# Kernel optimization log

Measured on AMD Instinct MI355X. Metric: run time of the kernel, lower is better.

The kernel has to match this reference:

```python
import jax, jax.numpy as jnp
import numpy as np

B, L, F, P, E, H, D, C, V = 256, 100, 8, 4, 64, 4, 64, 32, 10000
HD = H * D  # 256 = att_dim * head_num
TOWER_IN = F * E + F * E + P * E + C  # 1312
LN_EPS = 1e-3  # keras LayerNormalization default epsilon


def _ln(x, g, b):
    m = jnp.mean(x, axis=-1, keepdims=True)
    v = jnp.mean(jnp.square(x - m), axis=-1, keepdims=True)
    return (x - m) * jax.lax.rsqrt(v + LN_EPS) * g + b


def setup_inputs() -> dict:
    key = jax.random.key(0)
    ks = jax.random.split(key, 32)
    w = lambda k, s: jax.random.normal(k, s, jnp.float32) * 0.02
    inp = {
        'target_ad': jax.random.randint(ks[0], (B, F), 0, V),
        'ubs_feature': jax.random.randint(ks[1], (B, L, F), 0, V),
        'profile_feature': jax.random.randint(ks[2], (B, P), 0, V),
        'context_feature': jax.random.normal(ks[3], (B, C), jnp.float32),
        # embedding tables: one per sparse feature, stacked
        'item_tables': w(ks[4], (F, V, E)),
        'profile_tables': w(ks[5], (P, V, E)),
        # per-timestep distinct attention weights, stacked over L
        'q_w': w(ks[6], (L, E, HD)),
        'k_w': w(ks[7], (L, E, HD)),
        'v_w': w(ks[8], (L, E, HD)),
        'lin_w': w(ks[9], (L, HD, E)),
        'lin_b': jnp.zeros((L, E), jnp.float32),
        # shared post-attention layernorm
        'ln_g': jnp.ones((E,), jnp.float32),
        'ln_b': jnp.zeros((E,), jnp.float32),
        # dense tower
        't_w1': w(ks[10], (TOWER_IN, 1024)), 't_b1': jnp.zeros((1024,), jnp.float32),
        't_g1': jnp.ones((1024,), jnp.float32), 't_bb1': jnp.zeros((1024,), jnp.float32),
        't_w2': w(ks[11], (1024, 512)), 't_b2': jnp.zeros((512,), jnp.float32),
        't_g2': jnp.ones((512,), jnp.float32), 't_bb2': jnp.zeros((512,), jnp.float32),
        't_w3': w(ks[12], (512, 256)), 't_b3': jnp.zeros((256,), jnp.float32),
        't_g3': jnp.ones((256,), jnp.float32), 't_bb3': jnp.zeros((256,), jnp.float32),
        't_w4': w(ks[13], (256, 1)), 't_b4': jnp.zeros((1,), jnp.float32),
    }
    return inp


def reference(target_ad, ubs_feature, profile_feature, context_feature,
              item_tables, profile_tables, q_w, k_w, v_w, lin_w, lin_b,
              ln_g, ln_b,
              t_w1, t_b1, t_g1, t_bb1,
              t_w2, t_b2, t_g2, t_bb2,
              t_w3, t_b3, t_g3, t_bb3,
              t_w4, t_b4):
    b = target_ad.shape[0]
    # embedding lookups (feature-wise tables)
    te = item_tables[jnp.arange(F)[None, :], target_ad]              # [B,F,E]
    ue = item_tables[jnp.arange(F)[None, None, :], ubs_feature]      # [B,L,F,E]
    pe = profile_tables[jnp.arange(P)[None, :], profile_feature]     # [B,P,E]

    # per-step distinct Q/K/V projections, batched over L via einsum
    q = jnp.einsum('blfe,leo->blfo', ue, q_w).reshape(b, L, F, H, D)
    k = jnp.einsum('blfe,leo->blfo', ue, k_w).reshape(b, L, F, H, D)
    v = jnp.einsum('blfe,leo->blfo', ue, v_w).reshape(b, L, F, H, D)
    scores = jnp.einsum('blfhd,blghd->blhfg', q, k) / jnp.sqrt(jnp.float32(D))
    attw = jax.nn.softmax(scores, axis=-1)                           # [B,L,H,F,F]
    att = jnp.einsum('blhfg,blghd->blfhd', attw, v).reshape(b, L, F, HD)
    att_out = jnp.einsum('blfo,loe->blfe', att, lin_w) + lin_b[None, :, None, :]
    # shared LayerNorm per step, summed over L (original accumulates into zeros_like)
    ubs_t = jnp.sum(_ln(att_out, ln_g, ln_b), axis=1)                # [B,F,E]
    ubs = jax.nn.relu(ubs_t / jnp.float32(L))

    total = jnp.concatenate([ubs.reshape(b, -1), te.reshape(b, -1),
                             pe.reshape(b, -1), context_feature], axis=-1)

    h = jax.nn.relu(_ln(total @ t_w1 + t_b1, t_g1, t_bb1))
    h = jax.nn.relu(_ln(h @ t_w2 + t_b2, t_g2, t_bb2))
    h = jax.nn.relu(_ln(h @ t_w3 + t_b3, t_g3, t_bb3))
    out = jax.nn.sigmoid(h @ t_w4 + t_b4)                            # [B,1]
    return out
```

## Files before the change

### kernel.cpp

```cpp
#include <hip/hip_runtime.h>
#include <hip/hip_bf16.h>

#define B_ 256
#define L_ 100
#define F_ 8
#define P_ 4
#define E_ 64
#define H_ 4
#define D_ 64
#define C_ 32
#define V_ 10000
#define TOWER_IN_ 1312
#define LN_EPS 0.001f
#define LCH_ 4
#define NCH_ 25
#define ZK_ 40

typedef __attribute__((ext_vector_type(8))) short bf8v;
typedef __attribute__((ext_vector_type(8))) unsigned short us8;
typedef __attribute__((ext_vector_type(4))) float f4v;

__device__ __forceinline__ unsigned short f2bf(float x) {
    __hip_bfloat16 h = __float2bfloat16(x);
    return __builtin_bit_cast(unsigned short, h);
}

#define BARRIER() do { \
    asm volatile("s_waitcnt lgkmcnt(0)" ::: "memory"); \
    __builtin_amdgcn_s_barrier(); \
    asm volatile("" ::: "memory"); \
} while (0)

__global__ __launch_bounds__(256) void precomp_kernel(
    const float* __restrict__ q_w, const float* __restrict__ k_w,
    const float* __restrict__ v_w, const float* __restrict__ lin_w,
    unsigned short* __restrict__ wsMT, unsigned short* __restrict__ wsWT)
{
    __shared__ float sA[64][65];
    __shared__ float sB[64][65];
    const int t = threadIdx.x;
    const int l = blockIdx.x >> 2;
    const int h = blockIdx.x & 3;
    const size_t obase = (size_t)(l * 4 + h) * 4096;

    for (int i = 0; i < 16; ++i) {
        int idx = t + i * 256;
        int e = idx >> 6, d = idx & 63;
        sA[e][d] = q_w[(l * 64 + e) * 256 + h * 64 + d];
        sB[e][d] = k_w[(l * 64 + e) * 256 + h * 64 + d];
    }
    __syncthreads();
    for (int i = 0; i < 16; ++i) {
        int idx = t + i * 256;
        int o = idx >> 6, e = idx & 63;
        float s = 0.f;
        #pragma unroll 8
        for (int d = 0; d < 64; ++d) s += sA[e][d] * sB[o][d];
        wsMT[obase + idx] = f2bf(s);
    }
    __syncthreads();

    for (int i = 0; i < 16; ++i) {
        int idx = t + i * 256;
        int dd = idx >> 6, oo = idx & 63;
        sB[dd][oo] = lin_w[l * 16384 + (h * 64 + dd) * 64 + oo];
    }
    for (int i = 0; i < 16; ++i) {
        int idx = t + i * 256;
        int e = idx >> 6, d = idx & 63;
        sA[e][d] = v_w[(l * 64 + e) * 256 + h * 64 + d];
    }
    __syncthreads();
    for (int i = 0; i < 16; ++i) {
        int idx = t + i * 256;
        int o = idx >> 6, e = idx & 63;
        float s = 0.f;
        #pragma unroll 8
        for (int d = 0; d < 64; ++d) s += sA[e][d] * sB[d][o];
        wsWT[obase + idx] = f2bf(s);
    }
}

__global__ __launch_bounds__(256) void prep_kernel(
    const float* __restrict__ w1, const float* __restrict__ w2,
    const float* __restrict__ w3,
    unsigned short* __restrict__ Wt1, unsigned short* __restrict__ Wt2,
    unsigned short* __restrict__ Wt3)
{
    __shared__ float tile[32][33];
    int bx = blockIdx.x;
    const float* src; unsigned short* dst; int K, N, tk, tn;
    if (bx < 1312)      { src = w1; dst = Wt1; K = 1312; N = 1024; tk = bx / 32;  tn = bx % 32; }
    else if (bx < 1824) { int i = bx - 1312; src = w2; dst = Wt2; K = 1024; N = 512; tk = i / 16; tn = i % 16; }
    else                { int i = bx - 1824; src = w3; dst = Wt3; K = 512;  N = 256; tk = i / 8;  tn = i % 8; }
    const int k0 = tk * 32, n0 = tn * 32;
    const int rr = threadIdx.x >> 5, cc = threadIdx.x & 31;
    #pragma unroll
    for (int i = 0; i < 4; ++i) {
        int r = rr * 4 + i;
        tile[r][cc] = src[(size_t)(k0 + r) * N + n0 + cc];
    }
    __syncthreads();
    #pragma unroll
    for (int i = 0; i < 4; ++i) {
        int r = rr * 4 + i;
        dst[(size_t)(n0 + r) * K + k0 + cc] = f2bf(tile[cc][r]);
    }
}

__global__ __launch_bounds__(256, 3) void attn_kernel(
    const int* __restrict__ ubs_feature, const float* __restrict__ item_tables,
    const unsigned short* __restrict__ wsMT, const unsigned short* __restrict__ wsWT,
    const float* __restrict__ lin_b, const float* __restrict__ ln_g,
    const float* __restrict__ ln_b, float* __restrict__ ubs_acc)
{
    __shared__ __align__(16) unsigned short sUE[64][72];
    __shared__ __align__(16) unsigned short sT[64][136];
    __shared__ __align__(16) unsigned short sZt[4][64][ZK_];
    __shared__ __align__(16) unsigned short sAblk[4][16][32];
    __shared__ float sLng[64], sLnb[64], sLinb[LCH_][64];

    const int t = threadIdx.x;
    const int c = blockIdx.x >> 5;
    const int b0 = (blockIdx.x & 31) * 8;
    const int wv = t >> 6, lane = t & 63, quad = lane >> 4, cl = lane & 15;
    const int role = wv >> 1, hlw = wv & 1;

    const int grow = wv * 16 + (lane >> 2);
    const int gseg = lane & 3;
    const int gb = b0 + (grow >> 3), gf = grow & 7;

    if (t < 64) { sLng[t] = ln_g[t]; sLnb[t] = ln_b[t]; }
    if (t >= 64 && t < 128) {
        #pragma unroll
        for (int li = 0; li < LCH_; ++li)
            sLinb[li][t - 64] = lin_b[(c * LCH_ + li) * 64 + (t - 64)];
    }

    int vidx[LCH_];
    #pragma unroll
    for (int li = 0; li < LCH_; ++li)
        vidx[li] = ubs_feature[(gb * L_ + c * LCH_ + li) * F_ + gf];

    float4 pf[4];
    bf8v bfrag[4][2];

    auto load_bfrag = [&](int lh) {
        const unsigned short* Bsrc = (role == 0 ? wsMT : wsWT) + ((size_t)lh * 4096);
        #pragma unroll
        for (int nt = 0; nt < 4; ++nt)
            #pragma unroll
            for (int k2 = 0; k2 < 2; ++k2)
                bfrag[nt][k2] = *(const bf8v*)(Bsrc + (nt * 16 + cl) * 64 + k2 * 32 + quad * 8);
    };
    auto load_pf = [&](int li) {
        const float* srcp = item_tables + ((size_t)gf * V_ + vidx[li]) * 64 + gseg * 16;
        #pragma unroll
        for (int j = 0; j < 4; ++j) pf[j] = ((const float4*)srcp)[j];
    };
    auto store_ue = [&]() {
        us8 u0, u1;
        u0[0] = f2bf(pf[0].x); u0[1] = f2bf(pf[0].y); u0[2] = f2bf(pf[0].z); u0[3] = f2bf(pf[0].w);
        u0[4] = f2bf(pf[1].x); u0[5] = f2bf(pf[1].y); u0[6] = f2bf(pf[1].z); u0[7] = f2bf(pf[1].w);
        u1[0] = f2bf(pf[2].x); u1[1] = f2bf(pf[2].y); u1[2] = f2bf(pf[2].z); u1[3] = f2bf(pf[2].w);
        u1[4] = f2bf(pf[3].x); u1[5] = f2bf(pf[3].y); u1[6] = f2bf(pf[3].z); u1[7] = f2bf(pf[3].w);
        *(us8*)&sUE[grow][gseg * 16]     = u0;
        *(us8*)&sUE[grow][gseg * 16 + 8] = u1;
    };

    load_pf(0);
    load_bfrag((c * LCH_) * 4 + hlw);
    store_ue();
    BARRIER();

    float lnacc[16];
    #pragma unroll
    for (int i = 0; i < 16; ++i) lnacc[i] = 0.f;

    for (int li = 0; li < LCH_; ++li) {
        const int l = c * LCH_ + li;

        if (li + 1 < LCH_) load_pf(li + 1);

        f4v accO[4];
        #pragma unroll
        for (int nt = 0; nt < 4; ++nt) accO[nt] = {0.f, 0.f, 0.f, 0.f};

        #pragma unroll
        for (int half = 0; half < 2; ++half) {
            #pragma unroll
            for (int m = 0; m < 4; ++m) {
                bf8v a0 = *(const bf8v*)&sUE[m * 16 + cl][quad * 8];
                bf8v a1 = *(const bf8v*)&sUE[m * 16 + cl][32 + quad * 8];
                #pragma unroll
                for (int nt = 0; nt < 4; ++nt) {
                    f4v acc = {0.f, 0.f, 0.f, 0.f};
                    acc = __builtin_amdgcn_mfma_f32_16x16x32_bf16(a0, bfrag[nt][0], acc, 0, 0, 0);
                    acc = __builtin_amdgcn_mfma_f32_16x16x32_bf16(a1, bfrag[nt][1], acc, 0, 0, 0);
                    if (role == 0) {
                        #pragma unroll
                        for (int j = 0; j < 4; ++j)
                            sT[m * 16 + quad * 4 + j][hlw * 64 + nt * 16 + cl] = f2bf(acc[j]);
                    } else {
                        ushort4 zp;
                        zp.x = f2bf(acc[0]); zp.y = f2bf(acc[1]);
                        zp.z = f2bf(acc[2]); zp.w = f2bf(acc[3]);
                        const int k0 = (quad >> 1) * 16 + hlw * 8 + (quad & 1) * 4;
                        *(ushort4*)&sZt[m][nt * 16 + cl][k0] = zp;
                    }
                }
            }
            if (half == 0)            load_bfrag(l * 4 + 2 + hlw);
            else if (li + 1 < LCH_)   load_bfrag((l + 1) * 4 + hlw);
            BARRIER();

            {
                const int p = wv;
                const bool valid = (cl >> 3) == (quad >> 1);
                #pragma unroll
                for (int hl = 0; hl < 2; ++hl) {
                    bf8v a0s = *(const bf8v*)&sT[p * 16 + cl][hl * 64 + quad * 8];
                    bf8v a1s = *(const bf8v*)&sT[p * 16 + cl][hl * 64 + 32 + quad * 8];
                    bf8v u0 = *(const bf8v*)&sUE[p * 16 + cl][quad * 8];
                    bf8v u1 = *(const bf8v*)&sUE[p * 16 + cl][32 + quad * 8];
                    f4v acc = {0.f, 0.f, 0.f, 0.f};
                    acc = __builtin_amdgcn_mfma_f32_16x16x32_bf16(a0s, u0, acc, 0, 0, 0);
                    acc = __builtin_amdgcn_mfma_f32_16x16x32_bf16(a1s, u1, acc, 0, 0, 0);
                    const int kk = hl * 8 + (cl & 7) + (cl >> 3) * 16;
                    #pragma unroll
                    for (int j = 0; j < 4; ++j) {
                        float v = acc[j] * 0.125f;
                        float mx = v;
                        mx = fmaxf(mx, __shfl_xor(mx, 1));
                        mx = fmaxf(mx, __shfl_xor(mx, 2));
                        mx = fmaxf(mx, __shfl_xor(mx, 4));
                        float ex = __expf(v - mx);
                        float sm = ex;
                        sm += __shfl_xor(sm, 1);
                        sm += __shfl_xor(sm, 2);
                        sm += __shfl_xor(sm, 4);
                        float aw = valid ? ex * __builtin_amdgcn_rcpf(sm) : 0.f;
                        sAblk[p][quad * 4 + j][kk] = f2bf(aw);
                    }
                }
            }

            {
                const int p = wv;
                bf8v a0p = *(const bf8v*)&sAblk[p][cl][quad * 8];
                #pragma unroll
                for (int nt = 0; nt < 4; ++nt) {
                    bf8v bz = *(const bf8v*)&sZt[p][nt * 16 + cl][quad * 8];
                    accO[nt] = __builtin_amdgcn_mfma_f32_16x16x32_bf16(a0p, bz, accO[nt], 0, 0, 0);
                }
            }
            BARRIER();
        }

        {
            float x[16];
            #pragma unroll
            for (int nt = 0; nt < 4; ++nt)
                #pragma unroll
                for (int j = 0; j < 4; ++j)
                    x[nt * 4 + j] = accO[nt][j] + sLinb[li][nt * 16 + cl];
            #pragma unroll
            for (int j = 0; j < 4; ++j) {
                float s = x[j] + x[4 + j] + x[8 + j] + x[12 + j];
                #pragma unroll
                for (int m = 1; m < 16; m <<= 1) s += __shfl_xor(s, m);
                float mean = s * (1.f / 64.f);
                float q = 0.f;
                #pragma unroll
                for (int nt = 0; nt < 4; ++nt) { float d = x[nt * 4 + j] - mean; q += d * d; }
                #pragma unroll
                for (int m = 1; m < 16; m <<= 1) q += __shfl_xor(q, m);
                float rst = rsqrtf(q * (1.f / 64.f) + LN_EPS);
                #pragma unroll
                for (int nt = 0; nt < 4; ++nt) {
                    int col = nt * 16 + cl;
                    lnacc[nt * 4 + j] += (x[nt * 4 + j] - mean) * rst * sLng[col] + sLnb[col];
                }
            }
        }

        if (li + 1 < LCH_) {
            store_ue();
            BARRIER();
        }
    }

    #pragma unroll
    for (int j = 0; j < 4; ++j) {
        const int row = wv * 16 + quad * 4 + j;
        const int b = b0 + (row >> 3), f = row & 7;
        #pragma unroll
        for (int nt = 0; nt < 4; ++nt)
            atomicAdd(&ubs_acc[(size_t)b * 512 + f * 64 + nt * 16 + cl], lnacc[nt * 4 + j]);
    }
}

__device__ __forceinline__ float block_reduce_sum(float v, float* sRed) {
    #pragma unroll
    for (int m = 1; m < 64; m <<= 1) v += __shfl_xor(v, m, 64);
    int wave = threadIdx.x >> 6, lane = threadIdx.x & 63;
    __syncthreads();
    if (lane == 0) sRed[wave] = v;
    __syncthreads();
    return sRed[0] + sRed[1] + sRed[2] + sRed[3];
}

__global__ __launch_bounds__(256) void reduceX_kernel(
    const float* __restrict__ ubs_acc,
    const int* __restrict__ target_ad, const int* __restrict__ profile_feature,
    const float* __restrict__ context,
    const float* __restrict__ item_tables, const float* __restrict__ profile_tables,
    unsigned short* __restrict__ X)
{
    const int b = blockIdx.x, t = threadIdx.x;
    const float2 v = *(const float2*)(ubs_acc + (size_t)b * 512 + t * 2);
    X[b * TOWER_IN_ + t * 2]     = f2bf(fmaxf(v.x * 0.01f, 0.f));
    X[b * TOWER_IN_ + t * 2 + 1] = f2bf(fmaxf(v.y * 0.01f, 0.f));
    for (int cc = 512 + t; cc < TOWER_IN_; cc += 256) {
        float x;
        if (cc < 1024) { int j = cc - 512, f = j >> 6, e = j & 63;
            x = item_tables[((size_t)f * V_ + target_ad[b * 8 + f]) * 64 + e]; }
        else if (cc < 1280) { int j = cc - 1024, pp = j >> 6, e = j & 63;
            x = profile_tables[((size_t)pp * V_ + profile_feature[b * 4 + pp]) * 64 + e]; }
        else x = context[b * 32 + (cc - 1280)];
        X[b * TOWER_IN_ + cc] = f2bf(x);
    }
}

__global__ __launch_bounds__(256) void gemm_kernel(
    const unsigned short* __restrict__ A, const unsigned short* __restrict__ Bw,
    const float* __restrict__ bias, float* __restrict__ C, int K, int N)
{
    const int t = threadIdx.x;
    const int wv = t >> 6, lane = t & 63, quad = lane >> 4, cl = lane & 15;
    const int n0 = blockIdx.x * 64 + wv * 16;
    const int m0 = blockIdx.y * 16;
    f4v acc0 = {0.f, 0.f, 0.f, 0.f};
    f4v acc1 = {0.f, 0.f, 0.f, 0.f};
    const unsigned short* arow = A + (size_t)(m0 + cl) * K + quad * 8;
    const unsigned short* brow = Bw + (size_t)(n0 + cl) * K + quad * 8;
    int k0 = 0;
    #pragma unroll 2
    for (; k0 + 64 <= K; k0 += 64) {
        bf8v a0 = *(const bf8v*)(arow + k0);
        bf8v b0 = *(const bf8v*)(brow + k0);
        bf8v a1 = *(const bf8v*)(arow + k0 + 32);
        bf8v b1 = *(const bf8v*)(brow + k0 + 32);
        acc0 = __builtin_amdgcn_mfma_f32_16x16x32_bf16(a0, b0, acc0, 0, 0, 0);
        acc1 = __builtin_amdgcn_mfma_f32_16x16x32_bf16(a1, b1, acc1, 0, 0, 0);
    }
    if (k0 < K) {
        bf8v a = *(const bf8v*)(arow + k0);
        bf8v b = *(const bf8v*)(brow + k0);
        acc0 = __builtin_amdgcn_mfma_f32_16x16x32_bf16(a, b, acc0, 0, 0, 0);
    }
    float bv = bias[n0 + cl];
    #pragma unroll
    for (int j = 0; j < 4; ++j)
        C[(size_t)(m0 + quad * 4 + j) * N + n0 + cl] = acc0[j] + acc1[j] + bv;
}

__global__ __launch_bounds__(256) void ln_relu_kernel(
    const float* __restrict__ C, const float* __restrict__ g,
    const float* __restrict__ bb, unsigned short* __restrict__ Hx, int N)
{
    __shared__ float sRed[4];
    const int b = blockIdx.x, t = threadIdx.x;
    float s = 0.f, s2 = 0.f;
    for (int j = t; j < N; j += 256) { float x = C[(size_t)b * N + j]; s += x; s2 += x * x; }
    s  = block_reduce_sum(s,  sRed);
    __syncthreads();
    s2 = block_reduce_sum(s2, sRed);
    float invN = 1.f / (float)N;
    float mean = s * invN;
    float var  = s2 * invN - mean * mean;
    float rst  = rsqrtf(fmaxf(var, 0.f) + LN_EPS);
    for (int j = t; j < N; j += 256) {
        float x = C[(size_t)b * N + j];
        Hx[(size_t)b * N + j] = f2bf(fmaxf((x - mean) * rst * g[j] + bb[j], 0.f));
    }
}

__global__ __launch_bounds__(256) void final_kernel(
    const float* __restrict__ C3, const float* __restrict__ g3,
    const float* __restrict__ bb3, const float* __restrict__ w4,
    const float* __restrict__ b4, float* __restrict__ out)
{
    __shared__ float sRed[4];
    const int b = blockIdx.x, t = threadIdx.x;
    float x = C3[b * 256 + t];
    float s = block_reduce_sum(x, sRed);
    float mean = s * (1.f / 256.f);
    float d = x - mean;
    __syncthreads();
    float q = block_reduce_sum(d * d, sRed);
    float rst = rsqrtf(q * (1.f / 256.f) + LN_EPS);
    float h = fmaxf(d * rst * g3[t] + bb3[t], 0.f);
    __syncthreads();
    float p = block_reduce_sum(h * w4[t], sRed);
    if (t == 0) out[b] = 1.f / (1.f + expf(-(p + b4[0])));
}

extern "C" void kernel_launch(void* const* d_in, const int* in_sizes, int n_in,
                              void* d_out, int out_size, void* d_ws, size_t ws_size,
                              hipStream_t stream)
{
    (void)in_sizes; (void)n_in; (void)out_size; (void)ws_size;
    const int*   target_ad       = (const int*)d_in[0];
    const int*   ubs_feature     = (const int*)d_in[1];
    const int*   profile_feature = (const int*)d_in[2];
    const float* context         = (const float*)d_in[3];
    const float* item_tables     = (const float*)d_in[4];
    const float* profile_tables  = (const float*)d_in[5];
    const float* q_w   = (const float*)d_in[6];
    const float* k_w   = (const float*)d_in[7];
    const float* v_w   = (const float*)d_in[8];
    const float* lin_w = (const float*)d_in[9];
    const float* lin_b = (const float*)d_in[10];
    const float* ln_g  = (const float*)d_in[11];
    const float* ln_b  = (const float*)d_in[12];
    const float* t_w1  = (const float*)d_in[13];
    const float* t_b1  = (const float*)d_in[14];
    const float* t_g1  = (const float*)d_in[15];
    const float* t_bb1 = (const float*)d_in[16];
    const float* t_w2  = (const float*)d_in[17];
    const float* t_b2  = (const float*)d_in[18];
    const float* t_g2  = (const float*)d_in[19];
    const float* t_bb2 = (const float*)d_in[20];
    const float* t_w3  = (const float*)d_in[21];
    const float* t_b3  = (const float*)d_in[22];
    const float* t_g3  = (const float*)d_in[23];
    const float* t_bb3 = (const float*)d_in[24];
    const float* t_w4  = (const float*)d_in[25];
    const float* t_b4  = (const float*)d_in[26];

    char* ws = (char*)d_ws;
    unsigned short* wsMT = (unsigned short*)(ws);
    unsigned short* wsWT = (unsigned short*)(ws +  3276800);
    float* ubs_acc       = (float*)         (ws +  6553600);
    unsigned short* Wt1  = (unsigned short*)(ws +  7077888);
    unsigned short* Wt2  = (unsigned short*)(ws +  9764864);
    unsigned short* Wt3  = (unsigned short*)(ws + 10813440);
    unsigned short* X    = (unsigned short*)(ws + 11075584);
    float*          C1   = (float*)         (ws + 11747328);
    unsigned short* H1   = (unsigned short*)(ws + 12795904);
    float*          C2   = (float*)         (ws + 13320192);
    unsigned short* H2   = (unsigned short*)(ws + 13844480);
    float*          C3   = (float*)         (ws + 14106624);

    hipMemsetAsync(ubs_acc, 0, B_ * F_ * E_ * sizeof(float), stream);

    prep_kernel<<<1952, 256, 0, stream>>>(t_w1, t_w2, t_w3, Wt1, Wt2, Wt3);
    precomp_kernel<<<L_ * H_, 256, 0, stream>>>(q_w, k_w, v_w, lin_w, wsMT, wsWT);
    attn_kernel<<<NCH_ * 32, 256, 0, stream>>>(ubs_feature, item_tables, wsMT, wsWT,
                                               lin_b, ln_g, ln_b, ubs_acc);
    reduceX_kernel<<<B_, 256, 0, stream>>>(ubs_acc, target_ad, profile_feature, context,
                                           item_tables, profile_tables, X);
    gemm_kernel<<<dim3(16, 16), 256, 0, stream>>>(X,  Wt1, t_b1, C1, 1312, 1024);
    ln_relu_kernel<<<B_, 256, 0, stream>>>(C1, t_g1, t_bb1, H1, 1024);
    gemm_kernel<<<dim3(8, 16),  256, 0, stream>>>(H1, Wt2, t_b2, C2, 1024, 512);
    ln_relu_kernel<<<B_, 256, 0, stream>>>(C2, t_g2, t_bb2, H2, 512);
    gemm_kernel<<<dim3(4, 16),  256, 0, stream>>>(H2, Wt3, t_b3, C3, 512, 256);
    final_kernel<<<B_, 256, 0, stream>>>(C3, t_g3, t_bb3, t_w4, t_b4, (float*)d_out);
}
```

Measured before the change: 274.8 us.

## Fuse weight-prep kernels and whole dense tower into single kernels

```diff
diff --git a/kernel.cpp b/kernel.cpp
--- a/kernel.cpp
+++ b/kernel.cpp
@@ -31,80 +31,85 @@
     asm volatile("" ::: "memory"); \
 } while (0)
 
-__global__ __launch_bounds__(256) void precomp_kernel(
+__global__ __launch_bounds__(256) void prologue_kernel(
     const float* __restrict__ q_w, const float* __restrict__ k_w,
     const float* __restrict__ v_w, const float* __restrict__ lin_w,
-    unsigned short* __restrict__ wsMT, unsigned short* __restrict__ wsWT)
+    unsigned short* __restrict__ wsMT, unsigned short* __restrict__ wsWT,
+    const float* __restrict__ w1, const float* __restrict__ w2,
+    const float* __restrict__ w3,
+    unsigned short* __restrict__ Wt1, unsigned short* __restrict__ Wt2,
+    unsigned short* __restrict__ Wt3, float* __restrict__ ubs_acc)
 {
     __shared__ float sA[64][65];
     __shared__ float sB[64][65];
     const int t = threadIdx.x;
-    const int l = blockIdx.x >> 2;
-    const int h = blockIdx.x & 3;
-    const size_t obase = (size_t)(l * 4 + h) * 4096;
-
-    for (int i = 0; i < 16; ++i) {
-        int idx = t + i * 256;
-        int e = idx >> 6, d = idx & 63;
-        sA[e][d] = q_w[(l * 64 + e) * 256 + h * 64 + d];
-        sB[e][d] = k_w[(l * 64 + e) * 256 + h * 64 + d];
-    }
-    __syncthreads();
-    for (int i = 0; i < 16; ++i) {
-        int idx = t + i * 256;
-        int o = idx >> 6, e = idx & 63;
-        float s = 0.f;
-        #pragma unroll 8
-        for (int d = 0; d < 64; ++d) s += sA[e][d] * sB[o][d];
-        wsMT[obase + idx] = f2bf(s);
-    }
-    __syncthreads();
-
-    for (int i = 0; i < 16; ++i) {
-        int idx = t + i * 256;
-        int dd = idx >> 6, oo = idx & 63;
-        sB[dd][oo] = lin_w[l * 16384 + (h * 64 + dd) * 64 + oo];
-    }
-    for (int i = 0; i < 16; ++i) {
-        int idx = t + i * 256;
-        int e = idx >> 6, d = idx & 63;
-        sA[e][d] = v_w[(l * 64 + e) * 256 + h * 64 + d];
-    }
-    __syncthreads();
-    for (int i = 0; i < 16; ++i) {
-        int idx = t + i * 256;
-        int o = idx >> 6, e = idx & 63;
-        float s = 0.f;
-        #pragma unroll 8
-        for (int d = 0; d < 64; ++d) s += sA[e][d] * sB[d][o];
-        wsWT[obase + idx] = f2bf(s);
-    }
-}
-
-__global__ __launch_bounds__(256) void prep_kernel(
-    const float* __restrict__ w1, const float* __restrict__ w2,
-    const float* __restrict__ w3,
-    unsigned short* __restrict__ Wt1, unsigned short* __restrict__ Wt2,
-    unsigned short* __restrict__ Wt3)
-{
-    __shared__ float tile[32][33];
-    int bx = blockIdx.x;
-    const float* src; unsigned short* dst; int K, N, tk, tn;
-    if (bx < 1312)      { src = w1; dst = Wt1; K = 1312; N = 1024; tk = bx / 32;  tn = bx % 32; }
-    else if (bx < 1824) { int i = bx - 1312; src = w2; dst = Wt2; K = 1024; N = 512; tk = i / 16; tn = i % 16; }
-    else                { int i = bx - 1824; src = w3; dst = Wt3; K = 512;  N = 256; tk = i / 8;  tn = i % 8; }
-    const int k0 = tk * 32, n0 = tn * 32;
-    const int rr = threadIdx.x >> 5, cc = threadIdx.x & 31;
-    #pragma unroll
-    for (int i = 0; i < 4; ++i) {
-        int r = rr * 4 + i;
-        tile[r][cc] = src[(size_t)(k0 + r) * N + n0 + cc];
-    }
-    __syncthreads();
-    #pragma unroll
-    for (int i = 0; i < 4; ++i) {
-        int r = rr * 4 + i;
-        dst[(size_t)(n0 + r) * K + k0 + cc] = f2bf(tile[cc][r]);
+    const int bx = blockIdx.x;
+
+    if (bx < 400) {
+        const int l = bx >> 2;
+        const int h = bx & 3;
+        const size_t obase = (size_t)(l * 4 + h) * 4096;
+
+        for (int i = 0; i < 16; ++i) {
+            int idx = t + i * 256;
+            int e = idx >> 6, d = idx & 63;
+            sA[e][d] = q_w[(l * 64 + e) * 256 + h * 64 + d];
+            sB[e][d] = k_w[(l * 64 + e) * 256 + h * 64 + d];
+        }
+        __syncthreads();
+        for (int i = 0; i < 16; ++i) {
+            int idx = t + i * 256;
+            int o = idx >> 6, e = idx & 63;
+            float s = 0.f;
+            #pragma unroll 8
+            for (int d = 0; d < 64; ++d) s += sA[e][d] * sB[o][d];
+            wsMT[obase + idx] = f2bf(s);
+        }
+        __syncthreads();
+
+        for (int i = 0; i < 16; ++i) {
+            int idx = t + i * 256;
+            int dd = idx >> 6, oo = idx & 63;
+            sB[dd][oo] = lin_w[l * 16384 + (h * 64 + dd) * 64 + oo];
+        }
+        for (int i = 0; i < 16; ++i) {
+            int idx = t + i * 256;
+            int e = idx >> 6, d = idx & 63;
+            sA[e][d] = v_w[(l * 64 + e) * 256 + h * 64 + d];
+        }
+        __syncthreads();
+        for (int i = 0; i < 16; ++i) {
+            int idx = t + i * 256;
+            int o = idx >> 6, e = idx & 63;
+            float s = 0.f;
+            #pragma unroll 8
+            for (int d = 0; d < 64; ++d) s += sA[e][d] * sB[d][o];
+            wsWT[obase + idx] = f2bf(s);
+        }
+    } else if (bx < 2352) {
+        float (*tile)[65] = sA;
+        int bi = bx - 400;
+        const float* src; unsigned short* dst; int K, N, tk, tn;
+        if (bi < 1312)      { src = w1; dst = Wt1; K = 1312; N = 1024; tk = bi / 32;  tn = bi % 32; }
+        else if (bi < 1824) { int i = bi - 1312; src = w2; dst = Wt2; K = 1024; N = 512; tk = i / 16; tn = i % 16; }
+        else                { int i = bi - 1824; src = w3; dst = Wt3; K = 512;  N = 256; tk = i / 8;  tn = i % 8; }
+        const int k0 = tk * 32, n0 = tn * 32;
+        const int rr = t >> 5, cc = t & 31;
+        #pragma unroll
+        for (int i = 0; i < 4; ++i) {
+            int r = rr * 4 + i;
+            tile[r][cc] = src[(size_t)(k0 + r) * N + n0 + cc];
+        }
+        __syncthreads();
+        #pragma unroll
+        for (int i = 0; i < 4; ++i) {
+            int r = rr * 4 + i;
+            dst[(size_t)(n0 + r) * K + k0 + cc] = f2bf(tile[cc][r]);
+        }
+    } else {
+        const int bi = bx - 2352;
+        float4 z = {0.f, 0.f, 0.f, 0.f};
+        *(float4*)(ubs_acc + (size_t)bi * 1024 + t * 4) = z;
     }
 }
 
@@ -300,110 +305,208 @@
     }
 }
 
-__device__ __forceinline__ float block_reduce_sum(float v, float* sRed) {
-    #pragma unroll
-    for (int m = 1; m < 64; m <<= 1) v += __shfl_xor(v, m, 64);
-    int wave = threadIdx.x >> 6, lane = threadIdx.x & 63;
-    __syncthreads();
-    if (lane == 0) sRed[wave] = v;
-    __syncthreads();
-    return sRed[0] + sRed[1] + sRed[2] + sRed[3];
-}
-
-__global__ __launch_bounds__(256) void reduceX_kernel(
+#define TK1 1320
+#define TK2 1032
+#define TK3 520
+
+__global__ __launch_bounds__(1024) void tower_kernel(
     const float* __restrict__ ubs_acc,
     const int* __restrict__ target_ad, const int* __restrict__ profile_feature,
     const float* __restrict__ context,
     const float* __restrict__ item_tables, const float* __restrict__ profile_tables,
-    unsigned short* __restrict__ X)
+    const unsigned short* __restrict__ Wt1, const unsigned short* __restrict__ Wt2,
+    const unsigned short* __restrict__ Wt3,
+    const float* __restrict__ b1, const float* __restrict__ g1, const float* __restrict__ bb1,
+    const float* __restrict__ b2, const float* __restrict__ g2, const float* __restrict__ bb2,
+    const float* __restrict__ b3, const float* __restrict__ g3, const float* __restrict__ bb3,
+    const float* __restrict__ w4, const float* __restrict__ b4,
+    float* __restrict__ out)
 {
-    const int b = blockIdx.x, t = threadIdx.x;
-    const float2 v = *(const float2*)(ubs_acc + (size_t)b * 512 + t * 2);
-    X[b * TOWER_IN_ + t * 2]     = f2bf(fmaxf(v.x * 0.01f, 0.f));
-    X[b * TOWER_IN_ + t * 2 + 1] = f2bf(fmaxf(v.y * 0.01f, 0.f));
-    for (int cc = 512 + t; cc < TOWER_IN_; cc += 256) {
-        float x;
-        if (cc < 1024) { int j = cc - 512, f = j >> 6, e = j & 63;
-            x = item_tables[((size_t)f * V_ + target_ad[b * 8 + f]) * 64 + e]; }
-        else if (cc < 1280) { int j = cc - 1024, pp = j >> 6, e = j & 63;
-            x = profile_tables[((size_t)pp * V_ + profile_feature[b * 4 + pp]) * 64 + e]; }
-        else x = context[b * 32 + (cc - 1280)];
-        X[b * TOWER_IN_ + cc] = f2bf(x);
-    }
-}
-
-__global__ __launch_bounds__(256) void gemm_kernel(
-    const unsigned short* __restrict__ A, const unsigned short* __restrict__ Bw,
-    const float* __restrict__ bias, float* __restrict__ C, int K, int N)
-{
+    __shared__ __align__(16) char smem[61056];
+    unsigned short* sX  = (unsigned short*)smem;
+    unsigned short* sH1 = (unsigned short*)smem;
+    unsigned short* sH2 = (unsigned short*)(smem + 42240);
+    float* sRedS = (float*)(smem + 58880);
+    float* sRedQ = (float*)(smem + 59904);
+    float* sMean = (float*)(smem + 60928);
+    float* sRstd = (float*)(smem + 60992);
+
     const int t = threadIdx.x;
     const int wv = t >> 6, lane = t & 63, quad = lane >> 4, cl = lane & 15;
-    const int n0 = blockIdx.x * 64 + wv * 16;
-    const int m0 = blockIdx.y * 16;
-    f4v acc0 = {0.f, 0.f, 0.f, 0.f};
-    f4v acc1 = {0.f, 0.f, 0.f, 0.f};
-    const unsigned short* arow = A + (size_t)(m0 + cl) * K + quad * 8;
-    const unsigned short* brow = Bw + (size_t)(n0 + cl) * K + quad * 8;
-    int k0 = 0;
-    #pragma unroll 2
-    for (; k0 + 64 <= K; k0 += 64) {
-        bf8v a0 = *(const bf8v*)(arow + k0);
-        bf8v b0 = *(const bf8v*)(brow + k0);
-        bf8v a1 = *(const bf8v*)(arow + k0 + 32);
-        bf8v b1 = *(const bf8v*)(brow + k0 + 32);
-        acc0 = __builtin_amdgcn_mfma_f32_16x16x32_bf16(a0, b0, acc0, 0, 0, 0);
-        acc1 = __builtin_amdgcn_mfma_f32_16x16x32_bf16(a1, b1, acc1, 0, 0, 0);
-    }
-    if (k0 < K) {
-        bf8v a = *(const bf8v*)(arow + k0);
-        bf8v b = *(const bf8v*)(brow + k0);
-        acc0 = __builtin_amdgcn_mfma_f32_16x16x32_bf16(a, b, acc0, 0, 0, 0);
-    }
-    float bv = bias[n0 + cl];
-    #pragma unroll
-    for (int j = 0; j < 4; ++j)
-        C[(size_t)(m0 + quad * 4 + j) * N + n0 + cl] = acc0[j] + acc1[j] + bv;
-}
-
-__global__ __launch_bounds__(256) void ln_relu_kernel(
-    const float* __restrict__ C, const float* __restrict__ g,
-    const float* __restrict__ bb, unsigned short* __restrict__ Hx, int N)
-{
-    __shared__ float sRed[4];
-    const int b = blockIdx.x, t = threadIdx.x;
-    float s = 0.f, s2 = 0.f;
-    for (int j = t; j < N; j += 256) { float x = C[(size_t)b * N + j]; s += x; s2 += x * x; }
-    s  = block_reduce_sum(s,  sRed);
+    const int rb = blockIdx.x * 16;
+
+    {
+        const int r = wv;
+        const int gb = rb + r;
+        for (int cc = lane; cc < TOWER_IN_; cc += 64) {
+            float x;
+            if (cc < 512) x = fmaxf(ubs_acc[(size_t)gb * 512 + cc] * 0.01f, 0.f);
+            else if (cc < 1024) { int j = cc - 512, f = j >> 6, e = j & 63;
+                x = item_tables[((size_t)f * V_ + target_ad[gb * 8 + f]) * 64 + e]; }
+            else if (cc < 1280) { int j = cc - 1024, pp = j >> 6, e = j & 63;
+                x = profile_tables[((size_t)pp * V_ + profile_feature[gb * 4 + pp]) * 64 + e]; }
+            else x = context[gb * 32 + (cc - 1280)];
+            sX[r * TK1 + cc] = f2bf(x);
+        }
+    }
     __syncthreads();
-    s2 = block_reduce_sum(s2, sRed);
-    float invN = 1.f / (float)N;
-    float mean = s * invN;
-    float var  = s2 * invN - mean * mean;
-    float rst  = rsqrtf(fmaxf(var, 0.f) + LN_EPS);
-    for (int j = t; j < N; j += 256) {
-        float x = C[(size_t)b * N + j];
-        Hx[(size_t)b * N + j] = f2bf(fmaxf((x - mean) * rst * g[j] + bb[j], 0.f));
-    }
-}
-
-__global__ __launch_bounds__(256) void final_kernel(
-    const float* __restrict__ C3, const float* __restrict__ g3,
-    const float* __restrict__ bb3, const float* __restrict__ w4,
-    const float* __restrict__ b4, float* __restrict__ out)
-{
-    __shared__ float sRed[4];
-    const int b = blockIdx.x, t = threadIdx.x;
-    float x = C3[b * 256 + t];
-    float s = block_reduce_sum(x, sRed);
-    float mean = s * (1.f / 256.f);
-    float d = x - mean;
+
+    {
+        const int n0 = wv * 64;
+        f4v acc[4];
+        #pragma unroll
+        for (int nt = 0; nt < 4; ++nt) acc[nt] = {0.f, 0.f, 0.f, 0.f};
+        for (int k0 = 0; k0 < 1312; k0 += 32) {
+            bf8v a = *(const bf8v*)&sX[cl * TK1 + k0 + quad * 8];
+            #pragma unroll
+            for (int nt = 0; nt < 4; ++nt) {
+                bf8v b = *(const bf8v*)(Wt1 + (size_t)(n0 + nt * 16 + cl) * 1312 + k0 + quad * 8);
+                acc[nt] = __builtin_amdgcn_mfma_f32_16x16x32_bf16(a, b, acc[nt], 0, 0, 0);
+            }
+        }
+        #pragma unroll
+        for (int nt = 0; nt < 4; ++nt) {
+            float bv = b1[n0 + nt * 16 + cl];
+            #pragma unroll
+            for (int j = 0; j < 4; ++j) acc[nt][j] += bv;
+        }
+        #pragma unroll
+        for (int j = 0; j < 4; ++j) {
+            float s = acc[0][j] + acc[1][j] + acc[2][j] + acc[3][j];
+            float q = acc[0][j]*acc[0][j] + acc[1][j]*acc[1][j] + acc[2][j]*acc[2][j] + acc[3][j]*acc[3][j];
+            #pragma unroll
+            for (int m = 1; m < 16; m <<= 1) { s += __shfl_xor(s, m); q += __shfl_xor(q, m); }
+            if (cl == 0) { int row = quad * 4 + j; sRedS[row * 16 + wv] = s; sRedQ[row * 16 + wv] = q; }
+        }
+        __syncthreads();
+        if (t < 16) {
+            float s = 0.f, q = 0.f;
+            #pragma unroll
+            for (int w = 0; w < 16; ++w) { s += sRedS[t * 16 + w]; q += sRedQ[t * 16 + w]; }
+            float mean = s * (1.f / 1024.f);
+            float var  = q * (1.f / 1024.f) - mean * mean;
+            sMean[t] = mean;
+            sRstd[t] = rsqrtf(fmaxf(var, 0.f) + LN_EPS);
+        }
+        __syncthreads();
+        #pragma unroll
+        for (int nt = 0; nt < 4; ++nt) {
+            int col = n0 + nt * 16 + cl;
+            float gg = g1[col], bv = bb1[col];
+            #pragma unroll
+            for (int j = 0; j < 4; ++j) {
+                int row = quad * 4 + j;
+                float x = (acc[nt][j] - sMean[row]) * sRstd[row] * gg + bv;
+                sH1[row * TK2 + col] = f2bf(fmaxf(x, 0.f));
+            }
+        }
+    }
     __syncthreads();
-    float q = block_reduce_sum(d * d, sRed);
-    float rst = rsqrtf(q * (1.f / 256.f) + LN_EPS);
-    float h = fmaxf(d * rst * g3[t] + bb3[t], 0.f);
+
+    {
+        const int n0 = wv * 32;
+        f4v acc[2];
+        acc[0] = {0.f, 0.f, 0.f, 0.f}; acc[1] = {0.f, 0.f, 0.f, 0.f};
+        for (int k0 = 0; k0 < 1024; k0 += 32) {
+            bf8v a = *(const bf8v*)&sH1[cl * TK2 + k0 + quad * 8];
+            #pragma unroll
+            for (int nt = 0; nt < 2; ++nt) {
+                bf8v b = *(const bf8v*)(Wt2 + (size_t)(n0 + nt * 16 + cl) * 1024 + k0 + quad * 8);
+                acc[nt] = __builtin_amdgcn_mfma_f32_16x16x32_bf16(a, b, acc[nt], 0, 0, 0);
+            }
+        }
+        #pragma unroll
+        for (int nt = 0; nt < 2; ++nt) {
+            float bv = b2[n0 + nt * 16 + cl];
+            #pragma unroll
+            for (int j = 0; j < 4; ++j) acc[nt][j] += bv;
+        }
+        #pragma unroll
+        for (int j = 0; j < 4; ++j) {
+            float s = acc[0][j] + acc[1][j];
+            float q = acc[0][j]*acc[0][j] + acc[1][j]*acc[1][j];
+            #pragma unroll
+            for (int m = 1; m < 16; m <<= 1) { s += __shfl_xor(s, m); q += __shfl_xor(q, m); }
+            if (cl == 0) { int row = quad * 4 + j; sRedS[row * 16 + wv] = s; sRedQ[row * 16 + wv] = q; }
+        }
+        __syncthreads();
+        if (t < 16) {
+            float s = 0.f, q = 0.f;
+            #pragma unroll
+            for (int w = 0; w < 16; ++w) { s += sRedS[t * 16 + w]; q += sRedQ[t * 16 + w]; }
+            float mean = s * (1.f / 512.f);
+            float var  = q * (1.f / 512.f) - mean * mean;
+            sMean[t] = mean;
+            sRstd[t] = rsqrtf(fmaxf(var, 0.f) + LN_EPS);
+        }
+        __syncthreads();
+        #pragma unroll
+        for (int nt = 0; nt < 2; ++nt) {
+            int col = n0 + nt * 16 + cl;
+            float gg = g2[col], bv = bb2[col];
+            #pragma unroll
+            for (int j = 0; j < 4; ++j) {
+                int row = quad * 4 + j;
+                float x = (acc[nt][j] - sMean[row]) * sRstd[row] * gg + bv;
+                sH2[row * TK3 + col] = f2bf(fmaxf(x, 0.f));
+            }
+        }
+    }
     __syncthreads();
-    float p = block_reduce_sum(h * w4[t], sRed);
-    if (t == 0) out[b] = 1.f / (1.f + expf(-(p + b4[0])));
+
+    {
+        const int n0 = wv * 16;
+        f4v acc = {0.f, 0.f, 0.f, 0.f};
+        for (int k0 = 0; k0 < 512; k0 += 32) {
+            bf8v a = *(const bf8v*)&sH2[cl * TK3 + k0 + quad * 8];
+            bf8v b = *(const bf8v*)(Wt3 + (size_t)(n0 + cl) * 512 + k0 + quad * 8);
+            acc = __builtin_amdgcn_mfma_f32_16x16x32_bf16(a, b, acc, 0, 0, 0);
+        }
+        {
+            float bv = b3[n0 + cl];
+            #pragma unroll
+            for (int j = 0; j < 4; ++j) acc[j] += bv;
+        }
+        #pragma unroll
+        for (int j = 0; j < 4; ++j) {
+            float s = acc[j];
+            float q = acc[j] * acc[j];
+            #pragma unroll
+            for (int m = 1; m < 16; m <<= 1) { s += __shfl_xor(s, m); q += __shfl_xor(q, m); }
+            if (cl == 0) { int row = quad * 4 + j; sRedS[row * 16 + wv] = s; sRedQ[row * 16 + wv] = q; }
+        }
+        __syncthreads();
+        if (t < 16) {
+            float s = 0.f, q = 0.f;
+            #pragma unroll
+            for (int w = 0; w < 16; ++w) { s += sRedS[t * 16 + w]; q += sRedQ[t * 16 + w]; }
+            float mean = s * (1.f / 256.f);
+            float var  = q * (1.f / 256.f) - mean * mean;
+            sMean[t] = mean;
+            sRstd[t] = rsqrtf(fmaxf(var, 0.f) + LN_EPS);
+        }
+        __syncthreads();
+        {
+            int col = n0 + cl;
+            float gg = g3[col], bv = bb3[col], wv4 = w4[col];
+            #pragma unroll
+            for (int j = 0; j < 4; ++j) {
+                int row = quad * 4 + j;
+                float h = fmaxf((acc[j] - sMean[row]) * sRstd[row] * gg + bv, 0.f);
+                float p = h * wv4;
+                #pragma unroll
+                for (int m = 1; m < 16; m <<= 1) p += __shfl_xor(p, m);
+                if (cl == 0) sRedS[row * 16 + wv] = p;
+            }
+        }
+        __syncthreads();
+        if (t < 16) {
+            float p = 0.f;
+            #pragma unroll
+            for (int w = 0; w < 16; ++w) p += sRedS[t * 16 + w];
+            out[rb + t] = 1.f / (1.f + expf(-(p + b4[0])));
+        }
+    }
 }
 
 extern "C" void kernel_launch(void* const* d_in, const int* in_sizes, int n_in,
@@ -446,25 +549,13 @@
     unsigned short* Wt1  = (unsigned short*)(ws +  7077888);
     unsigned short* Wt2  = (unsigned short*)(ws +  9764864);
     unsigned short* Wt3  = (unsigned short*)(ws + 10813440);
-    unsigned short* X    = (unsigned short*)(ws + 11075584);
-    float*          C1   = (float*)         (ws + 11747328);
-    unsigned short* H1   = (unsigned short*)(ws + 12795904);
-    float*          C2   = (float*)         (ws + 13320192);
-    unsigned short* H2   = (unsigned short*)(ws + 13844480);
-    float*          C3   = (float*)         (ws + 14106624);
-
-    hipMemsetAsync(ubs_acc, 0, B_ * F_ * E_ * sizeof(float), stream);
-
-    prep_kernel<<<1952, 256, 0, stream>>>(t_w1, t_w2, t_w3, Wt1, Wt2, Wt3);
-    precomp_kernel<<<L_ * H_, 256, 0, stream>>>(q_w, k_w, v_w, lin_w, wsMT, wsWT);
+
+    prologue_kernel<<<2480, 256, 0, stream>>>(q_w, k_w, v_w, lin_w, wsMT, wsWT,
+                                              t_w1, t_w2, t_w3, Wt1, Wt2, Wt3, ubs_acc);
     attn_kernel<<<NCH_ * 32, 256, 0, stream>>>(ubs_feature, item_tables, wsMT, wsWT,
                                                lin_b, ln_g, ln_b, ubs_acc);
-    reduceX_kernel<<<B_, 256, 0, stream>>>(ubs_acc, target_ad, profile_feature, context,
-                                           item_tables, profile_tables, X);
-    gemm_kernel<<<dim3(16, 16), 256, 0, stream>>>(X,  Wt1, t_b1, C1, 1312, 1024);
-    ln_relu_kernel<<<B_, 256, 0, stream>>>(C1, t_g1, t_bb1, H1, 1024);
-    gemm_kernel<<<dim3(8, 16),  256, 0, stream>>>(H1, Wt2, t_b2, C2, 1024, 512);
-    ln_relu_kernel<<<B_, 256, 0, stream>>>(C2, t_g2, t_bb2, H2, 512);
-    gemm_kernel<<<dim3(4, 16),  256, 0, stream>>>(H2, Wt3, t_b3, C3, 512, 256);
-    final_kernel<<<B_, 256, 0, stream>>>(C3, t_g3, t_bb3, t_w4, t_b4, (float*)d_out);
+    tower_kernel<<<16, 1024, 0, stream>>>(ubs_acc, target_ad, profile_feature, context,
+                                          item_tables, profile_tables, Wt1, Wt2, Wt3,
+                                          t_b1, t_g1, t_bb1, t_b2, t_g2, t_bb2,
+                                          t_b3, t_g3, t_bb3, t_w4, t_b4, (float*)d_out);
 }
```

After: 340.7 us. +24.0%, slower.
